# Performance work log

Measured on AMD Instinct MI355X. Metric: run time of the kernel, lower is better.

The kernel has to match this reference:

```python
import jax, jax.numpy as jnp
import numpy as np

SMILE_LEN = 40


def _gru_cell(x, h, Wih, Whh, bih, bhh):
    # PyTorch GRU gate order: r, z, n
    gi = x @ Wih.T + bih          # [B, 3H]
    gh = h @ Whh.T + bhh          # [B, 3H]
    H = h.shape[-1]
    ir, iz, inn = gi[:, :H], gi[:, H:2 * H], gi[:, 2 * H:]
    hr, hz, hn = gh[:, :H], gh[:, H:2 * H], gh[:, 2 * H:]
    r = jax.nn.sigmoid(ir + hr)
    z = jax.nn.sigmoid(iz + hz)
    n = jnp.tanh(inn + r * hn)
    return (1.0 - z) * n + z * h


def setup_inputs() -> dict:
    key = jax.random.key(0)
    ks = jax.random.split(key, 12)
    B, L, H, A = 16384, 128, 256, 21
    s = 0.05
    return {
        "latent": jax.random.normal(ks[0], (B, L), jnp.float32),
        "W1": jax.random.normal(ks[1], (H, L), jnp.float32) * s,
        "b1": jax.random.normal(ks[2], (H,), jnp.float32) * s,
        "W2": jax.random.normal(ks[3], (H, H), jnp.float32) * s,
        "b2": jax.random.normal(ks[4], (H,), jnp.float32) * s,
        "Wih": jax.random.normal(ks[5], (3 * H, A), jnp.float32) * s,
        "Whh": jax.random.normal(ks[6], (3 * H, H), jnp.float32) * s,
        "bih": jax.random.normal(ks[7], (3 * H,), jnp.float32) * s,
        "bhh": jax.random.normal(ks[8], (3 * H,), jnp.float32) * s,
        "Wd": jax.random.normal(ks[9], (A, H), jnp.float32) * s,
        "bd": jax.random.normal(ks[10], (A,), jnp.float32) * s,
    }


def reference(latent, W1, b1, W2, b2, Wih, Whh, bih, bhh, Wd, bd):
    B = latent.shape[0]
    A = Wih.shape[1]
    # latent -> Dense -> ReLU -> (Dropout: identity in eval) -> Dense
    hidden = jax.nn.relu(latent @ W1.T + b1) @ W2.T + b2  # [B, H]
    # start token: +32 at position 0, -32 elsewhere
    start = jnp.full((B, A), -32.0, jnp.float32).at[:, 0].set(32.0)

    def step(carry, _):
        h, inp = carry
        h_new = _gru_cell(inp, h, Wih, Whh, bih, bhh)
        pred = h_new @ Wd.T + bd                      # [B, A]
        return (h_new, jax.lax.stop_gradient(pred)), pred

    (_, _), preds = jax.lax.scan(step, (hidden, start), None, length=SMILE_LEN - 1)
    # preds: [T-1, B, A] -> y: [B, T, A] with start token at t=0
    y = jnp.concatenate([start[:, None, :], jnp.transpose(preds, (1, 0, 2))], axis=1)
    return y
```

## Files before the change

kernel.cpp:

```cpp
#include <hip/hip_runtime.h>
#include <hip/hip_bf16.h>


typedef __bf16 bf16x8 __attribute__((ext_vector_type(8)));
typedef float  f32x16 __attribute__((ext_vector_type(16)));

#define MFMA32(a,b,c) __builtin_amdgcn_mfma_f32_32x32x16_bf16((a),(b),(c),0,0,0)
#define WAITV(n) asm volatile("s_waitcnt vmcnt(" #n ")" ::: "memory")
#define LGKM0()  asm volatile("s_waitcnt lgkmcnt(0)" ::: "memory")
#define BARRIER() do { asm volatile("" ::: "memory"); __builtin_amdgcn_s_barrier(); asm volatile("" ::: "memory"); } while (0)

static constexpr int A_DIM = 21;

static constexpr size_t O_W1F   = 0;
static constexpr size_t O_W2F   = O_W1F + 256*128*2;
static constexpr size_t O_ST1   = O_W2F + 256*256*2;
static constexpr size_t O_WMN   = O_ST1 + 8*16*3*1024;
static constexpr size_t O_WDF   = O_WMN + 8*16*4*1024;
static constexpr size_t O_BMAIN = O_WDF + 16*1024;
static constexpr size_t O_GI1   = O_BMAIN + 1024*4;


__global__ void prep_frag(const float* __restrict__ src, __bf16* __restrict__ dst,
                          int SR, int SC, int NF, int NCH) {
  int total = NF * NCH * 512;
  for (int i = blockIdx.x * blockDim.x + threadIdx.x; i < total;
       i += gridDim.x * blockDim.x) {
    int fragid = i >> 9, within = i & 511;
    int lane = within >> 3, j = within & 7;
    int nf = fragid / NCH, kc = fragid - nf * NCH;
    int n = nf * 32 + (lane & 31);
    int k = kc * 16 + (lane >> 5) * 8 + j;
    float v = (n < SR && k < SC) ? src[n * SC + k] : 0.f;
    dst[i] = (__bf16)v;
  }
}

__global__ void prep_st1(const float* __restrict__ Whh, __bf16* __restrict__ dst) {
  int total = 8 * 16 * 3 * 512;
  for (int i = blockIdx.x * blockDim.x + threadIdx.x; i < total;
       i += gridDim.x * blockDim.x) {
    int j = i & 7, lane = (i >> 3) & 63;
    int slice = i >> 9;
    int g = slice % 3, kc = (slice / 3) & 15, w = slice / 48;
    int n = g * 256 + w * 32 + (lane & 31);
    int k = kc * 16 + (lane >> 5) * 8 + j;
    dst[i] = (__bf16)Whh[n * 256 + k];
  }
}

__global__ void prep_main(const float* __restrict__ Whh, const float* __restrict__ Wih,
                          const float* __restrict__ Wd, __bf16* __restrict__ dst) {
  int total = 8 * 16 * 4 * 512;
  for (int i = blockIdx.x * blockDim.x + threadIdx.x; i < total;
       i += gridDim.x * blockDim.x) {
    int j = i & 7, lane = (i >> 3) & 63;
    int slice = i >> 9;
    int g = slice & 3, kc = (slice >> 2) & 15, w = slice >> 6;
    int k = kc * 16 + (lane >> 5) * 8 + j;
    int n = g * 256 + w * 32 + (lane & 31);
    float v = 0.f;
    if (n < 768) v = Whh[n * 256 + k];
    if (n < 512 || n >= 768) {
      int nn = (n < 512) ? n : (n - 256);
      float d = 0.f;
      #pragma unroll
      for (int q = 0; q < A_DIM; ++q) d += Wih[nn * A_DIM + q] * Wd[q * 256 + k];
      v += d;
    }
    dst[i] = (__bf16)v;
  }
}

__global__ void prep_bias(const float* __restrict__ Wih, const float* __restrict__ bih,
                          const float* __restrict__ bhh, const float* __restrict__ bd,
                          float* __restrict__ bmain, float* __restrict__ gi1c) {
  int i = blockIdx.x * blockDim.x + threadIdx.x;
  if (i < 1024) {
    float bm;
    if (i < 512) {
      float d = 0.f;
      #pragma unroll
      for (int q = 0; q < A_DIM; ++q) d += Wih[i * A_DIM + q] * bd[q];
      bm = bhh[i] + bih[i] + d;
    } else if (i < 768) {
      bm = bhh[i];
    } else {
      int nn = i - 256;
      float d = 0.f;
      #pragma unroll
      for (int q = 0; q < A_DIM; ++q) d += Wih[nn * A_DIM + q] * bd[q];
      bm = bih[nn] + d;
    }
    bmain[i] = bm;
  }
  if (i < 768) {
    float s = 32.f * Wih[i * A_DIM + 0];
    #pragma unroll
    for (int q = 1; q < A_DIM; ++q) s -= 32.f * Wih[i * A_DIM + q];
    gi1c[i] = s + bih[i];
  }
}


__device__ __forceinline__ void gload16(const void* g, void* l) {
  __builtin_amdgcn_global_load_lds((const __attribute__((address_space(1))) void*)g,
                                   (__attribute__((address_space(3))) void*)l, 16, 0, 0);
}

__device__ __forceinline__ bf16x8 lds_frag(const __bf16* base, int rowBytes,
                                           int row, int kb) {
  return *(const bf16x8*)((const char*)base + row * rowBytes +
                          (kb ^ ((row & 7) << 4)));
}

__device__ __forceinline__ void gru_gate(const f32x16& ar, const f32x16& az,
                                         const f32x16& ah, const f32x16& ai,
                                         f32x16& hr) {
  #pragma unroll
  for (int g = 0; g < 16; ++g) {
    float r = __builtin_amdgcn_rcpf(1.f + __builtin_amdgcn_exp2f(ar[g] * -1.442695041f));
    float z = __builtin_amdgcn_rcpf(1.f + __builtin_amdgcn_exp2f(az[g] * -1.442695041f));
    float pre = ai[g] + r * ah[g];
    float e = __builtin_amdgcn_exp2f(pre * 2.885390082f);
    float n = 1.f - 2.f * __builtin_amdgcn_rcpf(e + 1.f);
    hr[g] = n + z * (hr[g] - n);
  }
}

__device__ __forceinline__ void write_h(__bf16* hl, int c, int hfv,
                                        const f32x16& hr0, const f32x16& hr1) {
  #pragma unroll
  for (int g = 0; g < 16; ++g) {
    int pat = (g & 3) + 8 * (g >> 2) + 4 * hfv;
    int sw = (2 * c) ^ ((pat & 7) << 4);
    *(__bf16*)((char*)hl + pat * 512 + sw)        = (__bf16)hr0[g];
    *(__bf16*)((char*)hl + (32 + pat) * 512 + sw) = (__bf16)hr1[g];
  }
}

__global__ __launch_bounds__(512, 2) void decoder_main(
    const float* __restrict__ latent, const float* __restrict__ b1,
    const float* __restrict__ b2, const float* __restrict__ bhh,
    const float* __restrict__ bd, const float* __restrict__ gi1c,
    const float* __restrict__ bmain,
    const __bf16* __restrict__ W1f, const __bf16* __restrict__ W2f,
    const __bf16* __restrict__ St1, const __bf16* __restrict__ Wmn,
    const __bf16* __restrict__ Wdf, float* __restrict__ y) {
  __shared__ __attribute__((aligned(16))) __bf16 h_lds[64 * 256];
  __shared__ __attribute__((aligned(16))) char wd_lds[16 * 1024];
  __shared__ __attribute__((aligned(16))) char ringmem[8 * 3 * 4096];

  const int tid = threadIdx.x;
  const int w = tid >> 6;
  const int l = tid & 63;
  const int lc = l & 31;
  const int hfv = l >> 5;
  const int b0 = blockIdx.x * 64;
  const int c = w * 32 + lc;
  const int ph = (blockIdx.x >> 3) & 15;

  __bf16* lat_al = (__bf16*)(ringmem);
  __bf16* h1_al  = (__bf16*)(ringmem + 16384);

  for (int i = tid; i < 64 * A_DIM; i += 512) {
    int r = i / A_DIM, a = i - r * A_DIM;
    y[(size_t)(b0 + r) * 840 + a] = (a == 0) ? 32.f : -32.f;
  }

  for (int i = tid; i < 64 * 32; i += 512) {
    int r = i >> 5, c4 = i & 31;
    const float4 v = *(const float4*)(latent + (size_t)(b0 + r) * 128 + c4 * 4);
    __bf16* q = (__bf16*)((char*)lat_al + r * 256 + ((c4 * 8) ^ ((r & 7) << 4)));
    q[0] = (__bf16)v.x; q[1] = (__bf16)v.y; q[2] = (__bf16)v.z; q[3] = (__bf16)v.w;
  }
  __syncthreads();

  const bf16x8* W1v = (const bf16x8*)W1f;
  const bf16x8* W2v = (const bf16x8*)W2f;

  f32x16 acc0, acc1;
  {
    const float bb = b1[c];
    #pragma unroll
    for (int i = 0; i < 16; ++i) { acc0[i] = bb; acc1[i] = bb; }
  }
  #pragma unroll
  for (int kc = 0; kc < 8; ++kc) {
    bf16x8 a0 = lds_frag(lat_al, 256, lc, kc * 32 + hfv * 16);
    bf16x8 a1 = lds_frag(lat_al, 256, 32 + lc, kc * 32 + hfv * 16);
    bf16x8 bw = W1v[(w * 8 + kc) * 64 + l];
    acc0 = MFMA32(a0, bw, acc0);
    acc1 = MFMA32(a1, bw, acc1);
  }
  #pragma unroll
  for (int g = 0; g < 16; ++g) {
    int pat = (g & 3) + 8 * (g >> 2) + 4 * hfv;
    int sw = (2 * c) ^ ((pat & 7) << 4);
    float v0 = acc0[g] > 0.f ? acc0[g] : 0.f;
    float v1 = acc1[g] > 0.f ? acc1[g] : 0.f;
    *(__bf16*)((char*)h1_al + pat * 512 + sw)        = (__bf16)v0;
    *(__bf16*)((char*)h1_al + (32 + pat) * 512 + sw) = (__bf16)v1;
  }
  __syncthreads();

  f32x16 hr0, hr1;
  {
    const float bb = b2[c];
    #pragma unroll
    for (int i = 0; i < 16; ++i) { hr0[i] = bb; hr1[i] = bb; }
  }
  #pragma unroll
  for (int kc = 0; kc < 16; ++kc) {
    bf16x8 a0 = lds_frag(h1_al, 512, lc, kc * 32 + hfv * 16);
    bf16x8 a1 = lds_frag(h1_al, 512, 32 + lc, kc * 32 + hfv * 16);
    bf16x8 bw = W2v[(w * 16 + kc) * 64 + l];
    hr0 = MFMA32(a0, bw, hr0);
    hr1 = MFMA32(a1, bw, hr1);
  }
  write_h(h_lds, c, hfv, hr0, hr1);
  __syncthreads();

  const float i_r1 = bhh[c] + gi1c[c];
  const float i_z1 = bhh[256 + c] + gi1c[256 + c];
  const float i_h1 = bhh[512 + c];
  const float i_n1 = gi1c[512 + c];
  const float i_rm = bmain[c];
  const float i_zm = bmain[256 + c];
  const float i_hm = bmain[512 + c];
  const float i_nm = bmain[768 + c];
  const float pb = (lc < A_DIM) ? bd[lc] : 0.f;

  char* ringw = ringmem + w * 12288;
  const char* sW1 = (const char*)St1 + w * 49152 + (size_t)l * 16;
  const char* sW  = (const char*)Wmn + w * 65536 + (size_t)l * 16;

  gload16((const char*)Wdf + (w * 2 + 0) * 1024 + (size_t)l * 16, wd_lds + (w * 2 + 0) * 1024);
  gload16((const char*)Wdf + (w * 2 + 1) * 1024 + (size_t)l * 16, wd_lds + (w * 2 + 1) * 1024);

  f32x16 aR0, aR1, aZ0, aZ1, aH0, aH1, aI0, aI1, pacc;

  #pragma unroll
  for (int p = 0; p < 2; ++p)
    #pragma unroll
    for (int g = 0; g < 3; ++g)
      gload16(sW1 + ((p + ph) & 15) * 3072 + g * 1024, ringw + p * 4096 + g * 1024);

  #pragma unroll
  for (int i = 0; i < 16; ++i) {
    aR0[i] = i_r1; aR1[i] = i_r1; aZ0[i] = i_z1; aZ1[i] = i_z1;
    aH0[i] = i_h1; aH1[i] = i_h1; aI0[i] = i_n1; aI1[i] = i_n1;
  }
  #pragma unroll
  for (int kc = 0; kc < 16; ++kc) {
    const int kcp = (kc + ph) & 15;
    if (kc < 14) {
      const int fi = (kc + 2) % 3;
      const int kcp2 = (kc + 2 + ph) & 15;
      #pragma unroll
      for (int g = 0; g < 3; ++g)
        gload16(sW1 + kcp2 * 3072 + g * 1024, ringw + fi * 4096 + g * 1024);
    }
    if (kc < 14) { WAITV(6); } else if (kc == 14) { WAITV(3); } else { WAITV(0); }
    const char* fc = ringw + (kc % 3) * 4096 + (size_t)l * 16;
    bf16x8 a0 = lds_frag(h_lds, 512, lc, kcp * 32 + hfv * 16);
    bf16x8 a1 = lds_frag(h_lds, 512, 32 + lc, kcp * 32 + hfv * 16);
    bf16x8 br = *(const bf16x8*)(fc);
    bf16x8 bz = *(const bf16x8*)(fc + 1024);
    bf16x8 bh = *(const bf16x8*)(fc + 2048);
    aR0 = MFMA32(a0, br, aR0); aR1 = MFMA32(a1, br, aR1);
    aZ0 = MFMA32(a0, bz, aZ0); aZ1 = MFMA32(a1, bz, aZ1);
    aH0 = MFMA32(a0, bh, aH0); aH1 = MFMA32(a1, bh, aH1);
  }

  #pragma unroll
  for (int p = 0; p < 2; ++p) {
    const char* gsrc = sW + ((p + ph) & 15) * 4096;
    char* fd = ringw + p * 4096;
    gload16(gsrc,        fd);
    gload16(gsrc + 1024, fd + 1024);
    gload16(gsrc + 2048, fd + 2048);
    gload16(gsrc + 3072, fd + 3072);
  }

  gru_gate(aR0, aZ0, aH0, aI0, hr0);
  gru_gate(aR1, aZ1, aH1, aI1, hr1);
  LGKM0(); BARRIER();
  write_h(h_lds, c, hfv, hr0, hr1);
  LGKM0(); BARRIER();

  int base = 0;
  #pragma unroll 1
  for (int t = 2; t <= 39; ++t) {
    #pragma unroll
    for (int i = 0; i < 16; ++i) {
      aR0[i] = i_rm; aR1[i] = i_rm; aZ0[i] = i_zm; aZ1[i] = i_zm;
      aH0[i] = i_hm; aH1[i] = i_hm; aI0[i] = i_nm; aI1[i] = i_nm;
      pacc[i] = pb;
    }
    #pragma unroll
    for (int kc = 0; kc < 16; ++kc) {
      const int kcp = (kc + ph) & 15;
      {
        int f2 = (kc + 2) % 3 + base; if (f2 >= 3) f2 -= 3;
        const char* gsrc = sW + ((kc + 2 + ph) & 15) * 4096;
        char* fd = ringw + f2 * 4096;
        gload16(gsrc,        fd);
        gload16(gsrc + 1024, fd + 1024);
        gload16(gsrc + 2048, fd + 2048);
        gload16(gsrc + 3072, fd + 3072);
      }
      WAITV(8);
      int f0i = kc % 3 + base; if (f0i >= 3) f0i -= 3;
      const char* fc = ringw + f0i * 4096 + (size_t)l * 16;
      bf16x8 a0 = lds_frag(h_lds, 512, lc, kcp * 32 + hfv * 16);
      bf16x8 a1 = lds_frag(h_lds, 512, 32 + lc, kcp * 32 + hfv * 16);
      bf16x8 br = *(const bf16x8*)(fc);
      bf16x8 bz = *(const bf16x8*)(fc + 1024);
      bf16x8 bh = *(const bf16x8*)(fc + 2048);
      bf16x8 bi = *(const bf16x8*)(fc + 3072);
      aR0 = MFMA32(a0, br, aR0); aR1 = MFMA32(a1, br, aR1);
      aZ0 = MFMA32(a0, bz, aZ0); aZ1 = MFMA32(a1, bz, aZ1);
      aH0 = MFMA32(a0, bh, aH0); aH1 = MFMA32(a1, bh, aH1);
      aI0 = MFMA32(a0, bi, aI0); aI1 = MFMA32(a1, bi, aI1);
      if (w < 2) {
        bf16x8 bp = *(const bf16x8*)(wd_lds + kcp * 1024 + (size_t)l * 16);
        pacc = MFMA32(w ? a1 : a0, bp, pacc);
      }
    }
    if (w < 2 && lc < A_DIM) {
      #pragma unroll
      for (int g = 0; g < 16; ++g) {
        int pat = (g & 3) + 8 * (g >> 2) + 4 * hfv;
        y[(size_t)(b0 + 32 * w + pat) * 840 + (size_t)(t - 1) * 21 + lc] = pacc[g];
      }
    }
    gru_gate(aR0, aZ0, aH0, aI0, hr0);
    gru_gate(aR1, aZ1, aH1, aI1, hr1);
    LGKM0(); BARRIER();
    write_h(h_lds, c, hfv, hr0, hr1);
    LGKM0(); BARRIER();
    base = (base == 2) ? 0 : base + 1;
  }

  if (w < 2) {
    #pragma unroll
    for (int i = 0; i < 16; ++i) pacc[i] = pb;
    #pragma unroll
    for (int kc = 0; kc < 16; ++kc) {
      bf16x8 a = lds_frag(h_lds, 512, 32 * w + lc, kc * 32 + hfv * 16);
      bf16x8 bp = *(const bf16x8*)(wd_lds + kc * 1024 + (size_t)l * 16);
      pacc = MFMA32(a, bp, pacc);
    }
    if (lc < A_DIM) {
      #pragma unroll
      for (int g = 0; g < 16; ++g) {
        int pat = (g & 3) + 8 * (g >> 2) + 4 * hfv;
        y[(size_t)(b0 + 32 * w + pat) * 840 + 39 * 21 + lc] = pacc[g];
      }
    }
  }
  WAITV(0);
}

extern "C" void kernel_launch(void* const* d_in, const int* in_sizes, int n_in,
                              void* d_out, int out_size, void* d_ws, size_t ws_size,
                              hipStream_t stream) {
  const float* latent = (const float*)d_in[0];
  const float* W1 = (const float*)d_in[1];
  const float* b1 = (const float*)d_in[2];
  const float* W2 = (const float*)d_in[3];
  const float* b2 = (const float*)d_in[4];
  const float* Wih = (const float*)d_in[5];
  const float* Whh = (const float*)d_in[6];
  const float* bih = (const float*)d_in[7];
  const float* bhh = (const float*)d_in[8];
  const float* Wd = (const float*)d_in[9];
  const float* bd = (const float*)d_in[10];
  float* y = (float*)d_out;
  char* ws = (char*)d_ws;

  __bf16* W1f = (__bf16*)(ws + O_W1F);
  __bf16* W2f = (__bf16*)(ws + O_W2F);
  __bf16* St1 = (__bf16*)(ws + O_ST1);
  __bf16* Wmn = (__bf16*)(ws + O_WMN);
  __bf16* Wdf = (__bf16*)(ws + O_WDF);
  float* bmain = (float*)(ws + O_BMAIN);
  float* gi1c = (float*)(ws + O_GI1);

  prep_frag<<<128, 256, 0, stream>>>(W1, W1f, 256, 128, 8, 8);
  prep_frag<<<256, 256, 0, stream>>>(W2, W2f, 256, 256, 8, 16);
  prep_frag<<<32, 256, 0, stream>>>(Wd, Wdf, 21, 256, 1, 16);
  prep_st1<<<512, 256, 0, stream>>>(Whh, St1);
  prep_main<<<1024, 256, 0, stream>>>(Whh, Wih, Wd, Wmn);
  prep_bias<<<4, 256, 0, stream>>>(Wih, bih, bhh, bd, bmain, gi1c);

  decoder_main<<<256, 512, 0, stream>>>(latent, b1, b2, bhh, bd, gi1c, bmain,
                                        W1f, W2f, St1, Wmn, Wdf, y);
}
```

Baseline: 1.333 ms.

## Load GRU weights directly into registers and stage predictions through LDS

```diff
diff --git a/kernel.cpp b/kernel.cpp
--- a/kernel.cpp
+++ b/kernel.cpp
@@ -6,9 +6,6 @@
 typedef float  f32x16 __attribute__((ext_vector_type(16)));
 
 #define MFMA32(a,b,c) __builtin_amdgcn_mfma_f32_32x32x16_bf16((a),(b),(c),0,0,0)
-#define WAITV(n) asm volatile("s_waitcnt vmcnt(" #n ")" ::: "memory")
-#define LGKM0()  asm volatile("s_waitcnt lgkmcnt(0)" ::: "memory")
-#define BARRIER() do { asm volatile("" ::: "memory"); __builtin_amdgcn_s_barrier(); asm volatile("" ::: "memory"); } while (0)
 
 static constexpr int A_DIM = 21;
 
@@ -103,11 +100,6 @@
 }
 
 
-__device__ __forceinline__ void gload16(const void* g, void* l) {
-  __builtin_amdgcn_global_load_lds((const __attribute__((address_space(1))) void*)g,
-                                   (__attribute__((address_space(3))) void*)l, 16, 0, 0);
-}
-
 __device__ __forceinline__ bf16x8 lds_frag(const __bf16* base, int rowBytes,
                                            int row, int kb) {
   return *(const bf16x8*)((const char*)base + row * rowBytes +
@@ -148,8 +140,10 @@
     const __bf16* __restrict__ St1, const __bf16* __restrict__ Wmn,
     const __bf16* __restrict__ Wdf, float* __restrict__ y) {
   __shared__ __attribute__((aligned(16))) __bf16 h_lds[64 * 256];
+  __shared__ __attribute__((aligned(16))) __bf16 h1_lds[64 * 256];
+  __shared__ __attribute__((aligned(16))) __bf16 lat_lds[64 * 128];
   __shared__ __attribute__((aligned(16))) char wd_lds[16 * 1024];
-  __shared__ __attribute__((aligned(16))) char ringmem[8 * 3 * 4096];
+  __shared__ float pred_lds[2][64 * A_DIM];
 
   const int tid = threadIdx.x;
   const int w = tid >> 6;
@@ -160,19 +154,24 @@
   const int c = w * 32 + lc;
   const int ph = (blockIdx.x >> 3) & 15;
 
-  __bf16* lat_al = (__bf16*)(ringmem);
-  __bf16* h1_al  = (__bf16*)(ringmem + 16384);
-
   for (int i = tid; i < 64 * A_DIM; i += 512) {
     int r = i / A_DIM, a = i - r * A_DIM;
-    y[(size_t)(b0 + r) * 840 + a] = (a == 0) ? 32.f : -32.f;
+    __builtin_nontemporal_store((a == 0) ? 32.f : -32.f,
+                                &y[(size_t)(b0 + r) * 840 + a]);
   }
 
   for (int i = tid; i < 64 * 32; i += 512) {
     int r = i >> 5, c4 = i & 31;
     const float4 v = *(const float4*)(latent + (size_t)(b0 + r) * 128 + c4 * 4);
-    __bf16* q = (__bf16*)((char*)lat_al + r * 256 + ((c4 * 8) ^ ((r & 7) << 4)));
+    __bf16* q = (__bf16*)((char*)lat_lds + r * 256 + ((c4 * 8) ^ ((r & 7) << 4)));
     q[0] = (__bf16)v.x; q[1] = (__bf16)v.y; q[2] = (__bf16)v.z; q[3] = (__bf16)v.w;
+  }
+
+  {
+    bf16x8 v0 = *(const bf16x8*)((const char*)Wdf + (w * 2 + 0) * 1024 + (size_t)l * 16);
+    bf16x8 v1 = *(const bf16x8*)((const char*)Wdf + (w * 2 + 1) * 1024 + (size_t)l * 16);
+    *(bf16x8*)(wd_lds + (w * 2 + 0) * 1024 + (size_t)l * 16) = v0;
+    *(bf16x8*)(wd_lds + (w * 2 + 1) * 1024 + (size_t)l * 16) = v1;
   }
   __syncthreads();
 
@@ -187,8 +186,8 @@
   }
   #pragma unroll
   for (int kc = 0; kc < 8; ++kc) {
-    bf16x8 a0 = lds_frag(lat_al, 256, lc, kc * 32 + hfv * 16);
-    bf16x8 a1 = lds_frag(lat_al, 256, 32 + lc, kc * 32 + hfv * 16);
+    bf16x8 a0 = lds_frag(lat_lds, 256, lc, kc * 32 + hfv * 16);
+    bf16x8 a1 = lds_frag(lat_lds, 256, 32 + lc, kc * 32 + hfv * 16);
     bf16x8 bw = W1v[(w * 8 + kc) * 64 + l];
     acc0 = MFMA32(a0, bw, acc0);
     acc1 = MFMA32(a1, bw, acc1);
@@ -199,8 +198,8 @@
     int sw = (2 * c) ^ ((pat & 7) << 4);
     float v0 = acc0[g] > 0.f ? acc0[g] : 0.f;
     float v1 = acc1[g] > 0.f ? acc1[g] : 0.f;
-    *(__bf16*)((char*)h1_al + pat * 512 + sw)        = (__bf16)v0;
-    *(__bf16*)((char*)h1_al + (32 + pat) * 512 + sw) = (__bf16)v1;
+    *(__bf16*)((char*)h1_lds + pat * 512 + sw)        = (__bf16)v0;
+    *(__bf16*)((char*)h1_lds + (32 + pat) * 512 + sw) = (__bf16)v1;
   }
   __syncthreads();
 
@@ -212,8 +211,8 @@
   }
   #pragma unroll
   for (int kc = 0; kc < 16; ++kc) {
-    bf16x8 a0 = lds_frag(h1_al, 512, lc, kc * 32 + hfv * 16);
-    bf16x8 a1 = lds_frag(h1_al, 512, 32 + lc, kc * 32 + hfv * 16);
+    bf16x8 a0 = lds_frag(h1_lds, 512, lc, kc * 32 + hfv * 16);
+    bf16x8 a1 = lds_frag(h1_lds, 512, 32 + lc, kc * 32 + hfv * 16);
     bf16x8 bw = W2v[(w * 16 + kc) * 64 + l];
     hr0 = MFMA32(a0, bw, hr0);
     hr1 = MFMA32(a1, bw, hr1);
@@ -231,118 +230,131 @@
   const float i_nm = bmain[768 + c];
   const float pb = (lc < A_DIM) ? bd[lc] : 0.f;
 
-  char* ringw = ringmem + w * 12288;
   const char* sW1 = (const char*)St1 + w * 49152 + (size_t)l * 16;
   const char* sW  = (const char*)Wmn + w * 65536 + (size_t)l * 16;
-
-  gload16((const char*)Wdf + (w * 2 + 0) * 1024 + (size_t)l * 16, wd_lds + (w * 2 + 0) * 1024);
-  gload16((const char*)Wdf + (w * 2 + 1) * 1024 + (size_t)l * 16, wd_lds + (w * 2 + 1) * 1024);
+  #define S1F(kc) ((const bf16x8*)(sW1 + (((kc) + ph) & 15) * 3072))
+  #define SMF(kc) ((const bf16x8*)(sW  + (((kc) + ph) & 15) * 4096))
 
   f32x16 aR0, aR1, aZ0, aZ1, aH0, aH1, aI0, aI1, pacc;
-
-  #pragma unroll
-  for (int p = 0; p < 2; ++p)
-    #pragma unroll
-    for (int g = 0; g < 3; ++g)
-      gload16(sW1 + ((p + ph) & 15) * 3072 + g * 1024, ringw + p * 4096 + g * 1024);
-
-  #pragma unroll
-  for (int i = 0; i < 16; ++i) {
-    aR0[i] = i_r1; aR1[i] = i_r1; aZ0[i] = i_z1; aZ1[i] = i_z1;
-    aH0[i] = i_h1; aH1[i] = i_h1; aI0[i] = i_n1; aI1[i] = i_n1;
-  }
+  bf16x8 wA[4][2], wB[4][2];
+
+  #pragma unroll
+  for (int i = 0; i < 16; ++i) { aR0[i] = i_r1; aR1[i] = i_r1; aZ0[i] = i_z1; aZ1[i] = i_z1; }
+  wA[0][0] = S1F(0)[0];  wA[0][1] = S1F(0)[64];
+  wA[1][0] = S1F(1)[0];  wA[1][1] = S1F(1)[64];
   #pragma unroll
   for (int kc = 0; kc < 16; ++kc) {
+    if (kc < 14) {
+      wA[(kc + 2) & 3][0] = S1F(kc + 2)[0];
+      wA[(kc + 2) & 3][1] = S1F(kc + 2)[64];
+    } else {
+      wB[kc - 14][0] = S1F(kc - 14)[128];
+    }
     const int kcp = (kc + ph) & 15;
-    if (kc < 14) {
-      const int fi = (kc + 2) % 3;
-      const int kcp2 = (kc + 2 + ph) & 15;
-      #pragma unroll
-      for (int g = 0; g < 3; ++g)
-        gload16(sW1 + kcp2 * 3072 + g * 1024, ringw + fi * 4096 + g * 1024);
-    }
-    if (kc < 14) { WAITV(6); } else if (kc == 14) { WAITV(3); } else { WAITV(0); }
-    const char* fc = ringw + (kc % 3) * 4096 + (size_t)l * 16;
     bf16x8 a0 = lds_frag(h_lds, 512, lc, kcp * 32 + hfv * 16);
     bf16x8 a1 = lds_frag(h_lds, 512, 32 + lc, kcp * 32 + hfv * 16);
-    bf16x8 br = *(const bf16x8*)(fc);
-    bf16x8 bz = *(const bf16x8*)(fc + 1024);
-    bf16x8 bh = *(const bf16x8*)(fc + 2048);
-    aR0 = MFMA32(a0, br, aR0); aR1 = MFMA32(a1, br, aR1);
-    aZ0 = MFMA32(a0, bz, aZ0); aZ1 = MFMA32(a1, bz, aZ1);
-    aH0 = MFMA32(a0, bh, aH0); aH1 = MFMA32(a1, bh, aH1);
-  }
-
-  #pragma unroll
-  for (int p = 0; p < 2; ++p) {
-    const char* gsrc = sW + ((p + ph) & 15) * 4096;
-    char* fd = ringw + p * 4096;
-    gload16(gsrc,        fd);
-    gload16(gsrc + 1024, fd + 1024);
-    gload16(gsrc + 2048, fd + 2048);
-    gload16(gsrc + 3072, fd + 3072);
-  }
-
+    aR0 = MFMA32(a0, wA[kc & 3][0], aR0); aR1 = MFMA32(a1, wA[kc & 3][0], aR1);
+    aZ0 = MFMA32(a0, wA[kc & 3][1], aZ0); aZ1 = MFMA32(a1, wA[kc & 3][1], aZ1);
+  }
+  #pragma unroll
+  for (int i = 0; i < 16; ++i) { aH0[i] = i_h1; aH1[i] = i_h1; aI0[i] = i_n1; aI1[i] = i_n1; }
+  #pragma unroll
+  for (int kc = 0; kc < 16; ++kc) {
+    if (kc < 14) {
+      wB[(kc + 2) & 3][0] = S1F(kc + 2)[128];
+    } else {
+      wA[kc - 14][0] = SMF(kc - 14)[0];
+      wA[kc - 14][1] = SMF(kc - 14)[64];
+    }
+    const int kcp = (kc + ph) & 15;
+    bf16x8 a0 = lds_frag(h_lds, 512, lc, kcp * 32 + hfv * 16);
+    bf16x8 a1 = lds_frag(h_lds, 512, 32 + lc, kcp * 32 + hfv * 16);
+    aH0 = MFMA32(a0, wB[kc & 3][0], aH0); aH1 = MFMA32(a1, wB[kc & 3][0], aH1);
+  }
   gru_gate(aR0, aZ0, aH0, aI0, hr0);
   gru_gate(aR1, aZ1, aH1, aI1, hr1);
-  LGKM0(); BARRIER();
+  __syncthreads();
   write_h(h_lds, c, hfv, hr0, hr1);
-  LGKM0(); BARRIER();
-
-  int base = 0;
+  __syncthreads();
+
   #pragma unroll 1
   for (int t = 2; t <= 39; ++t) {
     #pragma unroll
-    for (int i = 0; i < 16; ++i) {
-      aR0[i] = i_rm; aR1[i] = i_rm; aZ0[i] = i_zm; aZ1[i] = i_zm;
-      aH0[i] = i_hm; aH1[i] = i_hm; aI0[i] = i_nm; aI1[i] = i_nm;
-      pacc[i] = pb;
-    }
+    for (int i = 0; i < 16; ++i) { aR0[i] = i_rm; aR1[i] = i_rm; aZ0[i] = i_zm; aZ1[i] = i_zm; }
     #pragma unroll
     for (int kc = 0; kc < 16; ++kc) {
+      if (kc < 14) {
+        wA[(kc + 2) & 3][0] = SMF(kc + 2)[0];
+        wA[(kc + 2) & 3][1] = SMF(kc + 2)[64];
+      } else {
+        wB[kc - 14][0] = SMF(kc - 14)[128];
+        wB[kc - 14][1] = SMF(kc - 14)[192];
+      }
       const int kcp = (kc + ph) & 15;
-      {
-        int f2 = (kc + 2) % 3 + base; if (f2 >= 3) f2 -= 3;
-        const char* gsrc = sW + ((kc + 2 + ph) & 15) * 4096;
-        char* fd = ringw + f2 * 4096;
-        gload16(gsrc,        fd);
-        gload16(gsrc + 1024, fd + 1024);
-        gload16(gsrc + 2048, fd + 2048);
-        gload16(gsrc + 3072, fd + 3072);
-      }
-      WAITV(8);
-      int f0i = kc % 3 + base; if (f0i >= 3) f0i -= 3;
-      const char* fc = ringw + f0i * 4096 + (size_t)l * 16;
       bf16x8 a0 = lds_frag(h_lds, 512, lc, kcp * 32 + hfv * 16);
       bf16x8 a1 = lds_frag(h_lds, 512, 32 + lc, kcp * 32 + hfv * 16);
-      bf16x8 br = *(const bf16x8*)(fc);
-      bf16x8 bz = *(const bf16x8*)(fc + 1024);
-      bf16x8 bh = *(const bf16x8*)(fc + 2048);
-      bf16x8 bi = *(const bf16x8*)(fc + 3072);
-      aR0 = MFMA32(a0, br, aR0); aR1 = MFMA32(a1, br, aR1);
-      aZ0 = MFMA32(a0, bz, aZ0); aZ1 = MFMA32(a1, bz, aZ1);
-      aH0 = MFMA32(a0, bh, aH0); aH1 = MFMA32(a1, bh, aH1);
-      aI0 = MFMA32(a0, bi, aI0); aI1 = MFMA32(a1, bi, aI1);
+      aR0 = MFMA32(a0, wA[kc & 3][0], aR0); aR1 = MFMA32(a1, wA[kc & 3][0], aR1);
+      aZ0 = MFMA32(a0, wA[kc & 3][1], aZ0); aZ1 = MFMA32(a1, wA[kc & 3][1], aZ1);
+    }
+    #pragma unroll
+    for (int i = 0; i < 16; ++i) { aH0[i] = i_hm; aH1[i] = i_hm; aI0[i] = i_nm; aI1[i] = i_nm; pacc[i] = pb; }
+    #pragma unroll
+    for (int kc = 0; kc < 16; ++kc) {
+      if (kc < 14) {
+        wB[(kc + 2) & 3][0] = SMF(kc + 2)[128];
+        wB[(kc + 2) & 3][1] = SMF(kc + 2)[192];
+      } else {
+        wA[kc - 14][0] = SMF(kc - 14)[0];
+        wA[kc - 14][1] = SMF(kc - 14)[64];
+      }
+      const int kcp = (kc + ph) & 15;
+      bf16x8 a0 = lds_frag(h_lds, 512, lc, kcp * 32 + hfv * 16);
+      bf16x8 a1 = lds_frag(h_lds, 512, 32 + lc, kcp * 32 + hfv * 16);
+      aH0 = MFMA32(a0, wB[kc & 3][0], aH0); aH1 = MFMA32(a1, wB[kc & 3][0], aH1);
+      aI0 = MFMA32(a0, wB[kc & 3][1], aI0); aI1 = MFMA32(a1, wB[kc & 3][1], aI1);
       if (w < 2) {
         bf16x8 bp = *(const bf16x8*)(wd_lds + kcp * 1024 + (size_t)l * 16);
         pacc = MFMA32(w ? a1 : a0, bp, pacc);
       }
     }
+    gru_gate(aR0, aZ0, aH0, aI0, hr0);
+    gru_gate(aR1, aZ1, aH1, aI1, hr1);
     if (w < 2 && lc < A_DIM) {
       #pragma unroll
       for (int g = 0; g < 16; ++g) {
         int pat = (g & 3) + 8 * (g >> 2) + 4 * hfv;
-        y[(size_t)(b0 + 32 * w + pat) * 840 + (size_t)(t - 1) * 21 + lc] = pacc[g];
-      }
-    }
-    gru_gate(aR0, aZ0, aH0, aI0, hr0);
-    gru_gate(aR1, aZ1, aH1, aI1, hr1);
-    LGKM0(); BARRIER();
+        pred_lds[(t - 1) & 1][(32 * w + pat) * A_DIM + lc] = pacc[g];
+      }
+    }
+    if (t >= 3) {
+      const float* ps = &pred_lds[t & 1][w * 8 * A_DIM];
+      #pragma unroll
+      for (int rep = 0; rep < 3; ++rep) {
+        int idx = rep * 64 + l;
+        if (idx < 8 * A_DIM) {
+          int rr = idx / A_DIM, cc = idx - rr * A_DIM;
+          __builtin_nontemporal_store(
+              ps[idx], &y[(size_t)(b0 + 8 * w + rr) * 840 + (size_t)(t - 2) * 21 + cc]);
+        }
+      }
+    }
+    __syncthreads();
     write_h(h_lds, c, hfv, hr0, hr1);
-    LGKM0(); BARRIER();
-    base = (base == 2) ? 0 : base + 1;
-  }
-
+    __syncthreads();
+  }
+
+  {
+    const float* ps = &pred_lds[0][w * 8 * A_DIM];
+    #pragma unroll
+    for (int rep = 0; rep < 3; ++rep) {
+      int idx = rep * 64 + l;
+      if (idx < 8 * A_DIM) {
+        int rr = idx / A_DIM, cc = idx - rr * A_DIM;
+        __builtin_nontemporal_store(
+            ps[idx], &y[(size_t)(b0 + 8 * w + rr) * 840 + (size_t)38 * 21 + cc]);
+      }
+    }
+  }
   if (w < 2) {
     #pragma unroll
     for (int i = 0; i < 16; ++i) pacc[i] = pb;
@@ -356,11 +368,13 @@
       #pragma unroll
       for (int g = 0; g < 16; ++g) {
         int pat = (g & 3) + 8 * (g >> 2) + 4 * hfv;
-        y[(size_t)(b0 + 32 * w + pat) * 840 + 39 * 21 + lc] = pacc[g];
-      }
-    }
-  }
-  WAITV(0);
+        __builtin_nontemporal_store(
+            pacc[g], &y[(size_t)(b0 + 32 * w + pat) * 840 + (size_t)39 * 21 + lc]);
+      }
+    }
+  }
+  #undef S1F
+  #undef SMF
 }
 
 extern "C" void kernel_launch(void* const* d_in, const int* in_sizes, int n_in,
```

Measured after the change: 1.473 ms. 10.5% more time.
